# Kernel tuning notes

Hardware: AMD Instinct MI355X
Metric: run time of the kernel (lower is better)

The kernel has to match this reference:

```python
import jax, jax.numpy as jnp
import numpy as np

M = 128  # template / canvas size (hardcoded in the module)


def _pair_indices(nodes_per_image):
    # Static (host-side) ragged pair construction, mirroring the Python loop
    # in the torch forward. Returns compressed index arrays for valid pairs.
    npi = np.asarray(nodes_per_image)
    idx_a, idx_b, batch, valid = [], [], [], []
    off = 0
    for b, n in enumerate(npi.tolist()):
        a = np.repeat(np.arange(n), n) + off   # repeat_interleave
        c = np.tile(np.arange(n), n) + off     # .repeat(n, 1)
        idx_a.append(a); idx_b.append(c)
        batch.append(np.full(n * n, b))
        if n > 1:
            v = np.triu(np.ones((n, n)), 1).astype(bool).reshape(-1)
        else:
            v = np.zeros((n * n,), bool)
        valid.append(v)
        off += n
    return (np.concatenate(idx_a), np.concatenate(idx_b),
            np.concatenate(batch), np.concatenate(valid))


def _grid_sample_bilinear(img, gx, gy):
    # img [O, M, M]; gx, gy [O, H, W] in [-1, 1]; align_corners=True, zero padding
    ix = (gx + 1.0) * 0.5 * (M - 1)
    iy = (gy + 1.0) * 0.5 * (M - 1)
    x0 = jnp.floor(ix); y0 = jnp.floor(iy)
    wx = ix - x0; wy = iy - y0
    out = jnp.zeros_like(gx)
    corners = ((0, 0, (1 - wy) * (1 - wx)), (0, 1, (1 - wy) * wx),
               (1, 0, wy * (1 - wx)), (1, 1, wy * wx))
    for dy, dx, w in corners:
        xi = x0 + dx; yi = y0 + dy
        inb = (xi >= 0) & (xi <= M - 1) & (yi >= 0) & (yi <= M - 1)
        xc = jnp.clip(xi, 0, M - 1).astype(jnp.int32)
        yc = jnp.clip(yi, 0, M - 1).astype(jnp.int32)
        v = jax.vmap(lambda m, yy, xx: m[yy, xx])(img, yc, xc)
        out = out + w * jnp.where(inb, v, 0.0)
    return out


def masks_to_layout(vecs, boxes, masks, obj_to_img, num_images, H):
    # sg2im-style: warp each mask into its box, scale by vec, scatter-add per image
    x0 = boxes[:, 0][:, None, None]; y0 = boxes[:, 1][:, None, None]
    x1 = boxes[:, 2][:, None, None]; y1 = boxes[:, 3][:, None, None]
    X = jnp.linspace(0.0, 1.0, H)[None, None, :]   # [1,1,W]
    Y = jnp.linspace(0.0, 1.0, H)[None, :, None]   # [1,H,1]
    gx = ((X - x0) / (x1 - x0)) * 2.0 - 1.0        # [O,1,W]
    gy = ((Y - y0) / (y1 - y0)) * 2.0 - 1.0        # [O,H,1]
    O = boxes.shape[0]
    gx = jnp.broadcast_to(gx, (O, H, H))
    gy = jnp.broadcast_to(gy, (O, H, H))
    sampled = _grid_sample_bilinear(masks, gx, gy)           # [O,H,W]
    sampled = sampled * vecs[:, 0][:, None, None]            # D = 1 channel
    out = jax.ops.segment_sum(sampled, obj_to_img, num_segments=num_images)
    return out[:, None]  # [B,1,H,W] (segment_sum already zero-pads empty images)


def _forward(nodes, adj_mat, nodes_per_image):
    ii = jnp.arange(M)
    # eye(128) max-pooled with k=11, s=1, p=5 -> band of half-width 10
    line_template = (jnp.abs(ii[:, None] - ii[None, :]) <= 10).astype(jnp.float32)
    idx_a, idx_b, batch_ids, valid = _pair_indices(nodes_per_image)
    sel = np.nonzero(valid)[0]
    idx_a = idx_a[sel]; idx_b = idx_b[sel]
    obj_to_img = jnp.asarray(batch_ids[sel], dtype=jnp.int32)
    boxes = jnp.concatenate([nodes[idx_a], nodes[idx_b]], axis=1)  # [O,4]
    vecs = adj_mat[sel]                                            # [O,1]
    B = int(np.asarray(nodes_per_image).shape[0])
    dual_slope = (jnp.abs((boxes[:, 3] - boxes[:, 1]) / (jnp.abs(boxes[:, 2] - boxes[:, 0]) + 1e-6))
                  + jnp.abs((boxes[:, 2] - boxes[:, 0]) / (jnp.abs(boxes[:, 3] - boxes[:, 1]) + 1e-6)))
    t = jnp.clip(2.0 * jax.nn.sigmoid(0.03 * (dual_slope - 2.0)) - 1.0, 0.0, 1.0)
    t = t[:, None, None]
    masks = (1.0 - t) * line_template[None, :, :] + t  # rect_template == ones
    img = masks_to_layout(vecs, boxes, masks, obj_to_img, B, M)
    return jnp.clip(img, 0.0, 1.0)


def setup_inputs() -> dict:
    key = jax.random.key(0)
    k1, k2 = jax.random.split(key)
    B, n = 24, 16
    nodes = jax.random.uniform(k1, (B * n, 2), dtype=jnp.float32)       # [384,2] in [0,1]
    adj_mat = jax.random.uniform(k2, (B * n * n, 1), dtype=jnp.float32)  # [6144,1]
    nodes_per_image = np.full((B,), n, dtype=np.int64)  # static ragged sizes
    return {"nodes": nodes, "adj_mat": adj_mat, "nodes_per_image": nodes_per_image}


def reference(nodes, adj_mat, nodes_per_image):
    return _forward(nodes, adj_mat, nodes_per_image)
```

## Files before the change

kernel.cpp:

```cpp
#include <hip/hip_runtime.h>

#define MM    128
#define NN    16
#define NPAIR 120
#define NIMG  24
#define ROWS  2
#define STRIPS 64
#define NWIN  4
#define CAP   121

__global__ __launch_bounds__(256) void g2i_kernel(
    const float* __restrict__ nodes,
    const float* __restrict__ adj,
    float* __restrict__ out)
{
    __shared__ float4 s_AB[NWIN][CAP * 4];
    __shared__ float  s_c [NWIN][CAP];
    __shared__ int    s_cnt[NWIN];

    const int img   = blockIdx.x >> 6;
    const int strip = (((blockIdx.x & 63) * 21) + img * 7) & 63;
    const int r0    = strip * ROWS;
    const int tid   = threadIdx.x;

    if (tid < NWIN) s_cnt[tid] = 0;
    __syncthreads();

    if (tid < NPAIR) {
        int k = tid, i = 0;
        while (k >= (NN - 1 - i)) { k -= (NN - 1 - i); ++i; }
        const int j = i + 1 + k;
        const float2 na = ((const float2*)nodes)[img * NN + i];
        const float2 nb = ((const float2*)nodes)[img * NN + j];
        const float x0 = na.x, y0 = na.y, x1 = nb.x, y1 = nb.y;
        const float dx = x1 - x0, dy = y1 - y0;

        const float ya  = 127.0f * y0 - dy;
        const float yb  = ya + 129.0f * dy;
        const float ylo = fminf(ya, yb) - 0.5f;
        const float yhi = fmaxf(ya, yb) + 0.5f;

        if (yhi >= (float)r0 && ylo <= (float)(r0 + ROWS - 1)) {
            const float adx = fabsf(dx), ady = fabsf(dy);
            const float ds  = ady * __builtin_amdgcn_rcpf(adx + 1e-6f)
                            + adx * __builtin_amdgcn_rcpf(ady + 1e-6f);
            const float e = __expf(-0.03f * (ds - 2.0f));
            float t = fmaf(2.0f, __builtin_amdgcn_rcpf(1.0f + e), -1.0f);
            t = fminf(fmaxf(t, 0.0f), 1.0f);
            const float vec = adj[img * NN * NN + i * NN + j];
            const float p = vec * t;
            const float q = vec * (1.0f - t);

            const float cax = __builtin_amdgcn_rcpf(dx);
            const float cbx = -127.0f * x0 * cax;
            const float cay = __builtin_amdgcn_rcpf(dy);
            const float cby = -127.0f * y0 * cay;

            float4 Ar[ROWS], Br[ROWS];
            #pragma unroll
            for (int r = 0; r < ROWS; ++r) {
                const float iy  = (float)(r0 + r) * cay + cby;
                const float y0f = floorf(iy);
                const float wy  = iy - y0f;
                const float ey0 = (y0f >=  0.0f && y0f <= 127.0f) ? (1.0f - wy) : 0.0f;
                const float ey1 = (y0f >= -1.0f && y0f <= 126.0f) ? wy          : 0.0f;
                const float A0 = fmaxf(0.0f,   y0f - 10.0f);
                const float B0 = fminf(127.0f, y0f + 10.0f);
                const float A1 = fmaxf(0.0f,   y0f -  9.0f);
                const float B1 = fminf(127.0f, y0f + 11.0f);
                Ar[r] = make_float4(-A0 + 1.0f, B0 - A0 + 2.0f,
                                    -A1 + 1.0f, B1 - A1 + 2.0f);
                Br[r] = make_float4(p * (ey0 + ey1), q * ey0, q * ey1, A0);
            }

            const float xa  = 127.0f * x0 - dx;
            const float xb  = xa + 129.0f * dx;
            const float xlo = fminf(xa, xb) - 0.5f;
            const float xhi = fmaxf(xa, xb) + 0.5f;

            #pragma unroll
            for (int w = 0; w < NWIN; ++w) {
                const float wl = (float)(w * 32) - 0.5f;
                const float wh = (float)(w * 32) + 31.5f;
                if (xhi >= wl && xlo <= wh) {
                    const int slot = atomicAdd(&s_cnt[w], 1);
                    const float base = fmaf((float)(w * 32), cax, cbx);
                    #pragma unroll
                    for (int r = 0; r < ROWS; ++r) {
                        s_AB[w][slot * 4 + r * 2 + 0] =
                            make_float4(base + Ar[r].x, Ar[r].y, base + Ar[r].z, Ar[r].w);
                        s_AB[w][slot * 4 + r * 2 + 1] = Br[r];
                    }
                    s_c[w][slot] = cax;
                }
            }
        }
    }
    __syncthreads();

    const int w    = tid >> 6;
    const int lane = tid & 63;
    const int lx   = lane & 31;
    const int row  = lane >> 5;
    const int px   = (w << 5) + lx;
    const int py   = r0 + row;
    const float fl = (float)lx;
    const int cnt  = s_cnt[w];

    const float4* __restrict__ AB = &s_AB[w][row * 2];
    const float*  __restrict__ C  = &s_c[w][0];

    float acc = 0.0f;
    float4 a_n = AB[0];
    float4 b_n = AB[1];
    float  c_n = C[0];

    for (int s = 0; s < cnt; ++s) {
        const float4 a = a_n;
        const float4 b = b_n;
        const float ca = c_n;
        a_n = AB[(s + 1) * 4 + 0];
        b_n = AB[(s + 1) * 4 + 1];
        c_n = C[s + 1];

        const float z0 = fmaf(fl, ca, a.x);
        const float s0 = a.y - z0;
        const float z1 = fmaf(fl, ca, a.z);
        const float s1 = a.w - z1;
        const float zs = z0 + b.w;
        const float t0 = __builtin_amdgcn_fmed3f(fminf(z0, s0), 0.0f, 1.0f);
        const float t1 = __builtin_amdgcn_fmed3f(fminf(z1, s1), 0.0f, 1.0f);
        const float ts = __builtin_amdgcn_fmed3f(fminf(zs, 129.0f - zs), 0.0f, 1.0f);
        acc = fmaf(b.x, ts, acc);
        acc = fmaf(b.y, t0, acc);
        acc = fmaf(b.z, t1, acc);
    }

    acc = fminf(fmaxf(acc, 0.0f), 1.0f);
    out[(size_t)img * (MM * MM) + py * MM + px] = acc;
}

extern "C" void kernel_launch(void* const* d_in, const int* in_sizes, int n_in,
                              void* d_out, int out_size, void* d_ws, size_t ws_size,
                              hipStream_t stream) {
    const float* nodes = (const float*)d_in[0];
    const float* adj   = (const float*)d_in[1];
    float* out = (float*)d_out;
    g2i_kernel<<<dim3(NIMG * STRIPS), dim3(256), 0, stream>>>(nodes, adj, out);
}
```

Before: 65.33 us.

## Use per-wave row/half-width segment lists with ballot-aggregated slot allocation

Each block now covers four rows split across two separated strips with 512 threads. Each wave owns one row and one 64-pixel half-width, and gets its own compacted segment list. List slots are allocated with a ballot and a single leader atomic per wave instead of per-thread LDS atomics. The pair index is now decoded with a closed-form sqrt instead of a loop. The intent is to halve setup per pixel, cut LDS atomic contention and shrink the per-wave list footprint, at the cost of more per-pair setup work and wider x-windows that may include more non-contributing segments.

```diff
diff --git a/kernel.cpp b/kernel.cpp
--- a/kernel.cpp
+++ b/kernel.cpp
@@ -1,35 +1,38 @@
 #include <hip/hip_runtime.h>
 
-#define MM    128
-#define NN    16
-#define NPAIR 120
-#define NIMG  24
-#define ROWS  2
-#define STRIPS 64
-#define NWIN  4
-#define CAP   121
+#define MM     128
+#define NN     16
+#define NPAIR  120
+#define NIMG   24
+#define BPI    32
+#define NLIST  8
+#define CAP    121
 
-__global__ __launch_bounds__(256) void g2i_kernel(
+__global__ __launch_bounds__(512, 6) void g2i_kernel(
     const float* __restrict__ nodes,
     const float* __restrict__ adj,
     float* __restrict__ out)
 {
-    __shared__ float4 s_AB[NWIN][CAP * 4];
-    __shared__ float  s_c [NWIN][CAP];
-    __shared__ int    s_cnt[NWIN];
+    __shared__ float4 s_AB[NLIST][CAP * 2];
+    __shared__ float  s_c [NLIST][CAP];
+    __shared__ int    s_cnt[NLIST];
 
-    const int img   = blockIdx.x >> 6;
-    const int strip = (((blockIdx.x & 63) * 21) + img * 7) & 63;
-    const int r0    = strip * ROWS;
-    const int tid   = threadIdx.x;
+    const int img  = blockIdx.x >> 5;
+    const int bp   = blockIdx.x & 31;
+    const int tid  = threadIdx.x;
+    const int lane = tid & 63;
 
-    if (tid < NWIN) s_cnt[tid] = 0;
+    if (tid < NLIST) s_cnt[tid] = 0;
     __syncthreads();
 
     if (tid < NPAIR) {
-        int k = tid, i = 0;
-        while (k >= (NN - 1 - i)) { k -= (NN - 1 - i); ++i; }
-        const int j = i + 1 + k;
+        const int k = tid;
+        int i = (int)(15.5f - sqrtf(240.25f - 2.0f * (float)k));
+        int oi = (i * (31 - i)) >> 1;
+        if (k < oi) { --i; oi = (i * (31 - i)) >> 1; }
+        else { const int oi1 = ((i + 1) * (30 - i)) >> 1; if (k >= oi1) { ++i; oi = oi1; } }
+        const int j = i + 1 + (k - oi);
+
         const float2 na = ((const float2*)nodes)[img * NN + i];
         const float2 nb = ((const float2*)nodes)[img * NN + j];
         const float x0 = na.x, y0 = na.y, x1 = nb.x, y1 = nb.y;
@@ -40,7 +43,12 @@
         const float ylo = fminf(ya, yb) - 0.5f;
         const float yhi = fmaxf(ya, yb) + 0.5f;
 
-        if (yhi >= (float)r0 && ylo <= (float)(r0 + ROWS - 1)) {
+        const float rA0 = (float)(2 * bp);
+        const float rB0 = (float)(2 * (bp + 32));
+        const bool anyy = ((yhi >= rA0 && ylo <= rA0 + 1.0f) ||
+                           (yhi >= rB0 && ylo <= rB0 + 1.0f));
+
+        if (anyy) {
             const float adx = fabsf(dx), ady = fabsf(dy);
             const float ds  = ady * __builtin_amdgcn_rcpf(adx + 1e-6f)
                             + adx * __builtin_amdgcn_rcpf(ady + 1e-6f);
@@ -48,79 +56,91 @@
             float t = fmaf(2.0f, __builtin_amdgcn_rcpf(1.0f + e), -1.0f);
             t = fminf(fmaxf(t, 0.0f), 1.0f);
             const float vec = adj[img * NN * NN + i * NN + j];
-            const float p = vec * t;
-            const float q = vec * (1.0f - t);
+            const float p = vec * t, q = vec * (1.0f - t);
 
             const float cax = __builtin_amdgcn_rcpf(dx);
             const float cbx = -127.0f * x0 * cax;
             const float cay = __builtin_amdgcn_rcpf(dy);
             const float cby = -127.0f * y0 * cay;
 
-            float4 Ar[ROWS], Br[ROWS];
-            #pragma unroll
-            for (int r = 0; r < ROWS; ++r) {
-                const float iy  = (float)(r0 + r) * cay + cby;
-                const float y0f = floorf(iy);
-                const float wy  = iy - y0f;
-                const float ey0 = (y0f >=  0.0f && y0f <= 127.0f) ? (1.0f - wy) : 0.0f;
-                const float ey1 = (y0f >= -1.0f && y0f <= 126.0f) ? wy          : 0.0f;
-                const float A0 = fmaxf(0.0f,   y0f - 10.0f);
-                const float B0 = fminf(127.0f, y0f + 10.0f);
-                const float A1 = fmaxf(0.0f,   y0f -  9.0f);
-                const float B1 = fminf(127.0f, y0f + 11.0f);
-                Ar[r] = make_float4(-A0 + 1.0f, B0 - A0 + 2.0f,
-                                    -A1 + 1.0f, B1 - A1 + 2.0f);
-                Br[r] = make_float4(p * (ey0 + ey1), q * ey0, q * ey1, A0);
-            }
-
             const float xa  = 127.0f * x0 - dx;
             const float xb  = xa + 129.0f * dx;
             const float xlo = fminf(xa, xb) - 0.5f;
             const float xhi = fmaxf(xa, xb) + 0.5f;
+            bool whit[2];
+            whit[0] = (xhi >= -0.5f) && (xlo <=  63.5f);
+            whit[1] = (xhi >= 63.5f) && (xlo <= 127.5f);
+            const float wb0 = cbx;
+            const float wb1 = fmaf(64.0f, cax, cbx);
 
             #pragma unroll
-            for (int w = 0; w < NWIN; ++w) {
-                const float wl = (float)(w * 32) - 0.5f;
-                const float wh = (float)(w * 32) + 31.5f;
-                if (xhi >= wl && xlo <= wh) {
-                    const int slot = atomicAdd(&s_cnt[w], 1);
-                    const float base = fmaf((float)(w * 32), cax, cbx);
+            for (int st = 0; st < 2; ++st) {
+                const float row0 = st ? rB0 : rA0;
+                #pragma unroll
+                for (int r = 0; r < 2; ++r) {
+                    const float ry = row0 + (float)r;
+                    const bool hy = (yhi >= ry) && (ylo <= ry);
+
+                    const float iy  = fmaf(ry, cay, cby);
+                    const float y0f = floorf(iy);
+                    const float wy  = iy - y0f;
+                    const float ey0 = (y0f >=  0.0f && y0f <= 127.0f) ? (1.0f - wy) : 0.0f;
+                    const float ey1 = (y0f >= -1.0f && y0f <= 126.0f) ? wy          : 0.0f;
+                    const float A0 = fmaxf(0.0f,   y0f - 10.0f);
+                    const float B0 = fminf(127.0f, y0f + 10.0f);
+                    const float A1 = fmaxf(0.0f,   y0f -  9.0f);
+                    const float B1 = fminf(127.0f, y0f + 11.0f);
+                    const float pe  = p * (ey0 + ey1);
+                    const float qe0 = q * ey0, qe1 = q * ey1;
+
                     #pragma unroll
-                    for (int r = 0; r < ROWS; ++r) {
-                        s_AB[w][slot * 4 + r * 2 + 0] =
-                            make_float4(base + Ar[r].x, Ar[r].y, base + Ar[r].z, Ar[r].w);
-                        s_AB[w][slot * 4 + r * 2 + 1] = Br[r];
+                    for (int w = 0; w < 2; ++w) {
+                        const bool hit = hy && whit[w];
+                        const unsigned long long m = __ballot(hit);
+                        if (m) {
+                            const int lid = st * 4 + w * 2 + r;
+                            const int leader = __ffsll(m) - 1;
+                            int base = 0;
+                            if (lane == leader) base = atomicAdd(&s_cnt[lid], (int)__popcll(m));
+                            base = __shfl(base, leader);
+                            if (hit) {
+                                const int slot = base + (int)__popcll(m & ((1ull << lane) - 1ull));
+                                const float wb = w ? wb1 : wb0;
+                                s_AB[lid][slot * 2 + 0] =
+                                    make_float4(wb + 1.0f - A0, B0 - A0 + 2.0f,
+                                                wb + 1.0f - A1, B1 - A1 + 2.0f);
+                                s_AB[lid][slot * 2 + 1] = make_float4(pe, qe0, qe1, A0);
+                                s_c [lid][slot] = cax;
+                            }
+                        }
                     }
-                    s_c[w][slot] = cax;
                 }
             }
         }
     }
     __syncthreads();
 
-    const int w    = tid >> 6;
-    const int lane = tid & 63;
-    const int lx   = lane & 31;
-    const int row  = lane >> 5;
-    const int px   = (w << 5) + lx;
-    const int py   = r0 + row;
-    const float fl = (float)lx;
-    const int cnt  = s_cnt[w];
+    const int wv = tid >> 6;
+    const int st = wv >> 2;
+    const int w  = (wv >> 1) & 1;
+    const int r  = wv & 1;
+    const int py = (st ? (bp + 32) : bp) * 2 + r;
+    const int px = w * 64 + lane;
+    const float fl = (float)lane;
+    const int cnt = s_cnt[wv];
 
-    const float4* __restrict__ AB = &s_AB[w][row * 2];
-    const float*  __restrict__ C  = &s_c[w][0];
+    const float4* __restrict__ AB = &s_AB[wv][0];
+    const float*  __restrict__ C  = &s_c[wv][0];
 
     float acc = 0.0f;
-    float4 a_n = AB[0];
-    float4 b_n = AB[1];
+    float4 a_n = AB[0], b_n = AB[1];
     float  c_n = C[0];
 
     for (int s = 0; s < cnt; ++s) {
-        const float4 a = a_n;
-        const float4 b = b_n;
+        const float4 a = a_n, b = b_n;
         const float ca = c_n;
-        a_n = AB[(s + 1) * 4 + 0];
-        b_n = AB[(s + 1) * 4 + 1];
+        a_n = AB[(s + 1) * 2 + 0];
+        b_n = AB[(s + 1) * 2 + 1];
         c_n = C[s + 1];
 
         const float z0 = fmaf(fl, ca, a.x);
@@ -146,5 +166,5 @@
     const float* nodes = (const float*)d_in[0];
     const float* adj   = (const float*)d_in[1];
     float* out = (float*)d_out;
-    g2i_kernel<<<dim3(NIMG * STRIPS), dim3(256), 0, stream>>>(nodes, adj, out);
+    g2i_kernel<<<dim3(NIMG * BPI), dim3(512), 0, stream>>>(nodes, adj, out);
 }
```

Measured after the change: 64.91 us. Within noise of the previous version (-0.6%).
